# Optimization experiments

Measured on AMD Instinct MI355X. Metric: run time of the kernel, lower is better.

## Reference

```python
import jax, jax.numpy as jnp
import numpy as np

B, T, W, F, H = 4, 1024, 33, 512, 8
DK = F // H


def setup_inputs() -> dict:
    key = jax.random.key(0)
    ks = jax.random.split(key, 12)
    s = 1.0 / np.sqrt(F)
    return {
        "query": jax.random.normal(ks[0], (B, T, F), jnp.float32),
        "key": jax.random.normal(ks[1], (B, T, W, F), jnp.float32),
        "value": jax.random.normal(ks[2], (B, T, W, F), jnp.float32),
        "mask": jnp.ones((B, 1, T, W), jnp.int32),
        "Wq": jax.random.uniform(ks[3], (F, F), jnp.float32, -s, s),
        "bq": jax.random.uniform(ks[4], (F,), jnp.float32, -s, s),
        "Wk": jax.random.uniform(ks[5], (F, F), jnp.float32, -s, s),
        "bk": jax.random.uniform(ks[6], (F,), jnp.float32, -s, s),
        "Wv": jax.random.uniform(ks[7], (F, F), jnp.float32, -s, s),
        "bv": jax.random.uniform(ks[8], (F,), jnp.float32, -s, s),
        "Wo": jax.random.uniform(ks[9], (F, F), jnp.float32, -s, s),
        "bo": jax.random.uniform(ks[10], (F,), jnp.float32, -s, s),
    }


def reference(query, key, value, mask, Wq, bq, Wk, bk, Wv, bv, Wo, bo):
    b, t, w, f = key.shape
    # projections
    q = (query @ Wq + bq).reshape(b, t, H, DK)            # (B,T,H,Dk)
    k = (key @ Wk + bk).reshape(b, t, w, H, DK)           # (B,T,W,H,Dk)
    v = (value @ Wv + bv).reshape(b, t, w, H, DK)
    # windowed scores: each query attends to its own window of keys
    scores = jnp.einsum("bthd,btwhd->bhtw", q, k) / jnp.sqrt(jnp.asarray(DK, q.dtype))
    m = (mask == 0)                                       # (B,1,T,W), broadcasts over heads
    min_value = jnp.finfo(scores.dtype).min
    scores = jnp.where(m, min_value, scores)
    attn = jax.nn.softmax(scores, axis=-1)
    attn = jnp.where(m, 0.0, attn)                        # (B,H,T,W)
    x = jnp.einsum("bhtw,btwhd->bthd", attn, v).reshape(b, t, H * DK)
    return x @ Wo + bo
```

## Files before the change

kernel.cpp:

```cpp
#include <hip/hip_runtime.h>
#include <hip/hip_bf16.h>
#include <cstdint>

#define B_ 4
#define T_ 1024
#define W_ 33
#define F_ 512
#define H_ 8
#define DK_ 64

typedef __attribute__((ext_vector_type(8))) short short8;
typedef __attribute__((ext_vector_type(4))) float f32x4;

__device__ __forceinline__ float b2f(ushort u) {
  return __uint_as_float(((uint32_t)u) << 16);
}
__device__ __forceinline__ ushort f2b(float f) {
  union { __hip_bfloat16 b; ushort u; } cv;
  cv.b = __float2bfloat16(f);
  return cv.u;
}

__global__ void convert_w(const float* __restrict__ Wq, const float* __restrict__ Wk,
                          const float* __restrict__ Wv, const float* __restrict__ Wo,
                          ushort* __restrict__ out)
{
  int which = blockIdx.y;
  const float* src = (which == 0) ? Wq : (which == 1) ? Wk : (which == 2) ? Wv : Wo;
  ushort* dst = out + (size_t)which * 262144;
  int idx = blockIdx.x * 256 + threadIdx.x;
  int e = idx & 7;
  int l = (idx >> 3) & 63;
  float v;
  if (which == 1) {
    int kc  = (idx >> 9) & 1;
    int ntf = (idx >> 10) & 31;
    int h   = idx >> 15;
    v = src[(size_t)(ntf * 16 + (l & 15)) * 512 + h * 64 + kc * 32 + ((l >> 4) << 3) + e];
  } else {
    int kc = (idx >> 9) & 15;
    int nt = idx >> 13;
    int k = kc * 32 + ((l >> 4) << 3) + e;
    int n = (nt << 4) + (l & 15);
    v = src[(size_t)k * 512 + n];
  }
  dst[idx] = f2b(v);
}

template<bool A_F32, bool OUT_F32>
__global__ __launch_bounds__(256, 2)
void gemm_pipe(const void* __restrict__ Ap, const ushort* __restrict__ Bf,
               const float* __restrict__ bias, void* __restrict__ Cp, float scale)
{
  __shared__ ushort lA[3][128 * 64];

  const int tid  = threadIdx.x;
  const int lane = tid & 63;
  const int wid  = tid >> 6;
  const int wr   = wid >> 1, wc = wid & 1;
  const int lrow = lane & 15;
  const int lk8  = (lane >> 4) * 8;

  int nwg  = gridDim.x;
  int xcd  = blockIdx.x & 7;
  int slot = blockIdx.x >> 3;
  int q8   = nwg >> 3, r8 = nwg & 7;
  int base = (xcd < r8) ? xcd * (q8 + 1) : r8 * (q8 + 1) + (xcd - r8) * q8;
  int L    = base + slot;
  int bm   = L >> 2;
  int bn   = L & 3;

  int lb_[4];
  size_t asrc_[4];
#pragma unroll
  for (int p = 0; p < 4; ++p) {
    int c   = p * 256 + tid;
    int row = c >> 3;
    int kc  = (c & 7) * 8;
    lb_[p]  = (row * 128 + kc * 2) ^ ((row & 7) << 4);
    asrc_[p] = (size_t)(bm * 128 + row) * 512 + kc;
  }

  const int ntb = bn * 8 + wc * 4;

  float4 P0a0[4], P0a1[4], P1a0[4], P1a1[4];
  short8 P0r[4], P1r[4];
  short8 Q0[8], Q1[8];

  auto issueA = [&](int ks, float4 (&d0)[4], float4 (&d1)[4], short8 (&dr)[4]) {
#pragma unroll
    for (int p = 0; p < 4; ++p) {
      if (A_F32) {
        const float* src = (const float*)Ap + asrc_[p] + ks * 64;
        d0[p] = *(const float4*)src;
        d1[p] = *(const float4*)(src + 4);
      } else {
        dr[p] = *(const short8*)((const ushort*)Ap + asrc_[p] + ks * 64);
      }
    }
  };
  auto lwriteA = [&](int buf, float4 (&d0)[4], float4 (&d1)[4], short8 (&dr)[4]) {
#pragma unroll
    for (int p = 0; p < 4; ++p) {
      short8 hv;
      if (A_F32) {
        hv[0] = (short)f2b(d0[p].x); hv[1] = (short)f2b(d0[p].y);
        hv[2] = (short)f2b(d0[p].z); hv[3] = (short)f2b(d0[p].w);
        hv[4] = (short)f2b(d1[p].x); hv[5] = (short)f2b(d1[p].y);
        hv[6] = (short)f2b(d1[p].z); hv[7] = (short)f2b(d1[p].w);
      } else {
        hv = dr[p];
      }
      *(short8*)((char*)lA[buf] + lb_[p]) = hv;
    }
  };
  auto loadB = [&](int ks, short8 (&dq)[8]) {
#pragma unroll
    for (int kk = 0; kk < 2; ++kk)
#pragma unroll
      for (int nf = 0; nf < 4; ++nf)
        dq[kk * 4 + nf] = *(const short8*)(Bf +
            (((size_t)(ntb + nf) * 16 + ks * 2 + kk) * 64 + lane) * 8);
  };

  f32x4 acc[4][4];
#pragma unroll
  for (int i = 0; i < 4; ++i)
#pragma unroll
    for (int j = 0; j < 4; ++j) acc[i][j] = {0.f, 0.f, 0.f, 0.f};

  auto computeStep = [&](int buf, short8 (&dq)[8]) {
#pragma unroll
    for (int kk = 0; kk < 2; ++kk) {
      short8 af[4];
#pragma unroll
      for (int mf = 0; mf < 4; ++mf) {
        int row = wr * 64 + mf * 16 + lrow;
        int off = (row * 128 + (kk * 32 + lk8) * 2) ^ ((row & 7) << 4);
        af[mf] = *(const short8*)((const char*)lA[buf] + off);
      }
#pragma unroll
      for (int mf = 0; mf < 4; ++mf)
#pragma unroll
        for (int nf = 0; nf < 4; ++nf)
          acc[mf][nf] = __builtin_amdgcn_mfma_f32_16x16x32_bf16(af[mf], dq[kk * 4 + nf], acc[mf][nf], 0, 0, 0);
    }
  };

  issueA(0, P0a0, P0a1, P0r);
  issueA(1, P1a0, P1a1, P1r);
  loadB(0, Q0);
  lwriteA(0, P0a0, P0a1, P0r);
  __syncthreads();

#define GSTEP(T, PWa0, PWa1, PWr, PIa0, PIa1, PIr, QW, QR)                    \
  {                                                                           \
    if ((T) + 1 < 8) lwriteA(((T) + 1) % 3, PWa0, PWa1, PWr);                 \
    if ((T) + 2 < 8) issueA((T) + 2, PIa0, PIa1, PIr);                        \
    if ((T) + 1 < 8) loadB((T) + 1, QW);                                      \
    computeStep((T) % 3, QR);                                                 \
    if ((T) < 7) __syncthreads();                                             \
  }

  GSTEP(0, P1a0, P1a1, P1r, P0a0, P0a1, P0r, Q1, Q0)
  GSTEP(1, P0a0, P0a1, P0r, P1a0, P1a1, P1r, Q0, Q1)
  GSTEP(2, P1a0, P1a1, P1r, P0a0, P0a1, P0r, Q1, Q0)
  GSTEP(3, P0a0, P0a1, P0r, P1a0, P1a1, P1r, Q0, Q1)
  GSTEP(4, P1a0, P1a1, P1r, P0a0, P0a1, P0r, Q1, Q0)
  GSTEP(5, P0a0, P0a1, P0r, P1a0, P1a1, P1r, Q0, Q1)
  GSTEP(6, P1a0, P1a1, P1r, P0a0, P0a1, P0r, Q1, Q0)
  GSTEP(7, P0a0, P0a1, P0r, P1a0, P1a1, P1r, Q0, Q1)
#undef GSTEP

  float bs[4];
#pragma unroll
  for (int nf = 0; nf < 4; ++nf)
    bs[nf] = bias[bn * 128 + wc * 64 + nf * 16 + lrow];

  const int r0 = (lane >> 4) * 4;
#pragma unroll
  for (int mf = 0; mf < 4; ++mf) {
#pragma unroll
    for (int nf = 0; nf < 4; ++nf) {
      int gcol = bn * 128 + wc * 64 + nf * 16 + lrow;
#pragma unroll
      for (int r = 0; r < 4; ++r) {
        int grow = bm * 128 + wr * 64 + mf * 16 + r0 + r;
        float val = (acc[mf][nf][r] + bs[nf]) * scale;
        if (OUT_F32) ((float*)Cp)[(size_t)grow * 512 + gcol] = val;
        else         ((ushort*)Cp)[(size_t)grow * 512 + gcol] = f2b(val);
      }
    }
  }
}

__global__ __launch_bounds__(256, 4)
void r_gemm(const ushort* __restrict__ q, const ushort* __restrict__ WkR,
            ushort* __restrict__ R)
{
  const int tid  = threadIdx.x;
  const int lane = tid & 63;
  const int wid  = tid >> 6;
  const int lr   = lane & 15;
  const int l8   = (lane >> 4) * 8;
  const int mg   = blockIdx.x >> 1;
  const int nh   = blockIdx.x & 1;
  const int h    = blockIdx.y;
  const int m0   = mg * 64;
  const int ntb  = nh * 16 + wid * 4;

  short8 af[2][4], bg[2][4];
#pragma unroll
  for (int ks = 0; ks < 2; ++ks)
#pragma unroll
    for (int mf = 0; mf < 4; ++mf)
      af[ks][mf] = *(const short8*)(q + (size_t)(m0 + mf * 16 + lr) * 512 + h * 64 + ks * 32 + l8);
#pragma unroll
  for (int ks = 0; ks < 2; ++ks)
#pragma unroll
    for (int nf = 0; nf < 4; ++nf)
      bg[ks][nf] = *(const short8*)(WkR + ((size_t)((h * 32 + ntb + nf) * 2 + ks) * 64 + lane) * 8);

  f32x4 acc[4][4];
#pragma unroll
  for (int i = 0; i < 4; ++i)
#pragma unroll
    for (int j = 0; j < 4; ++j) acc[i][j] = {0.f, 0.f, 0.f, 0.f};

#pragma unroll
  for (int ks = 0; ks < 2; ++ks)
#pragma unroll
    for (int mf = 0; mf < 4; ++mf)
#pragma unroll
      for (int nf = 0; nf < 4; ++nf)
        acc[mf][nf] = __builtin_amdgcn_mfma_f32_16x16x32_bf16(af[ks][mf], bg[ks][nf], acc[mf][nf], 0, 0, 0);

  const int rr = (lane >> 4) * 4;
#pragma unroll
  for (int mf = 0; mf < 4; ++mf)
#pragma unroll
    for (int nf = 0; nf < 4; ++nf) {
      int col = nh * 256 + wid * 64 + nf * 16 + lr;
#pragma unroll
      for (int r = 0; r < 4; ++r) {
        int row = m0 + mf * 16 + rr + r;
        R[((size_t)row * 8 + h) * 512 + col] = f2b(acc[mf][nf][r]);
      }
    }
}

__global__ __launch_bounds__(256, 6)
void attn_scores(const float* __restrict__ key, const ushort* __restrict__ R,
                 const int* __restrict__ mask, float* __restrict__ probs,
                 float* __restrict__ asum)
{
  __shared__ float la[W_][8];

  const int tid  = threadIdx.x;
  const int lane = tid & 63;
  const int wv   = tid >> 6;
  const int bt   = blockIdx.x;

  int mreg = 0;
  if (lane < W_) mreg = mask[(size_t)bt * W_ + lane];
  unsigned long long mbits = __ballot(mreg != 0);

  const int h0 = wv * 2;
  float Rf[2][8];
  {
    const ushort* Rb = R + (size_t)bt * 4096 + lane * 8;
    short8 rv0 = *(const short8*)(Rb + (size_t)h0 * 512);
    short8 rv1 = *(const short8*)(Rb + (size_t)(h0 + 1) * 512);
#pragma unroll
    for (int j = 0; j < 8; ++j) {
      Rf[0][j] = b2f((ushort)rv0[j]);
      Rf[1][j] = b2f((ushort)rv1[j]);
    }
  }

  const float* kb = key + (size_t)bt * (W_ * 512) + lane * 8;
#pragma unroll 3
  for (int w = 0; w < W_; ++w) {
    float4 ka = *(const float4*)(kb + (size_t)w * 512);
    float4 kc = *(const float4*)(kb + (size_t)w * 512 + 4);
    float s0 = ka.x * Rf[0][0] + ka.y * Rf[0][1] + ka.z * Rf[0][2] + ka.w * Rf[0][3]
             + kc.x * Rf[0][4] + kc.y * Rf[0][5] + kc.z * Rf[0][6] + kc.w * Rf[0][7];
    float s1 = ka.x * Rf[1][0] + ka.y * Rf[1][1] + ka.z * Rf[1][2] + ka.w * Rf[1][3]
             + kc.x * Rf[1][4] + kc.y * Rf[1][5] + kc.z * Rf[1][6] + kc.w * Rf[1][7];
#pragma unroll
    for (int m = 1; m < 64; m <<= 1) {
      s0 += __shfl_xor(s0, m, 64);
      s1 += __shfl_xor(s1, m, 64);
    }
    float t = (lane == 0) ? s0 : s1;
    float e = ((mbits >> w) & 1ull) ? __expf(t) : 0.f;
    if (lane < 2) la[w][h0 + lane] = e;
  }
  __syncthreads();

  const int hh = tid & 7;
  float ss = 0.f;
#pragma unroll
  for (int w = 0; w < W_; ++w) ss += la[w][hh];
  float inv = (mbits != 0ull) ? 1.f / ss : 0.f;

  for (int t = tid; t < H_ * W_; t += 256) {
    int w = t >> 3;
    probs[(size_t)bt * 264 + t] = la[w][hh] * inv;
  }
  if (tid < H_)
    asum[(size_t)bt * H_ + tid] = (mbits != 0ull) ? 1.f : 0.f;
}

__global__ __launch_bounds__(256, 8)
void attn_pv(const float* __restrict__ value, const float* __restrict__ probs,
             ushort* __restrict__ g)
{
  __shared__ float lp[W_ * 8];

  const int tid = threadIdx.x;
  const int bt  = blockIdx.x;

  for (int c = tid; c < W_ * 8; c += 256)
    lp[c] = probs[(size_t)bt * 264 + c];
  __syncthreads();

  const float* vb = value + (size_t)bt * (W_ * 512) + tid * 2;
  float gg0[8], gg1[8];
#pragma unroll
  for (int h = 0; h < 8; ++h) { gg0[h] = 0.f; gg1[h] = 0.f; }

#pragma unroll
  for (int w = 0; w < W_; ++w) {
    float2 v = *(const float2*)(vb + (size_t)w * 512);
    f32x4 a0 = *(const f32x4*)&lp[w * 8];
    f32x4 a1 = *(const f32x4*)&lp[w * 8 + 4];
    gg0[0] += a0[0] * v.x; gg1[0] += a0[0] * v.y;
    gg0[1] += a0[1] * v.x; gg1[1] += a0[1] * v.y;
    gg0[2] += a0[2] * v.x; gg1[2] += a0[2] * v.y;
    gg0[3] += a0[3] * v.x; gg1[3] += a0[3] * v.y;
    gg0[4] += a1[0] * v.x; gg1[4] += a1[0] * v.y;
    gg0[5] += a1[1] * v.x; gg1[5] += a1[1] * v.y;
    gg0[6] += a1[2] * v.x; gg1[6] += a1[2] * v.y;
    gg0[7] += a1[3] * v.x; gg1[7] += a1[3] * v.y;
  }

  ushort* gb = g + (size_t)bt * 4096 + tid * 2;
#pragma unroll
  for (int h = 0; h < 8; ++h) {
    ushort2 pk;
    pk.x = f2b(gg0[h]);
    pk.y = f2b(gg1[h]);
    *(ushort2*)(gb + h * 512) = pk;
  }
}

__global__ __launch_bounds__(256, 2)
void x_proj(const ushort* __restrict__ g, const ushort* __restrict__ WtV,
            const float* __restrict__ bv, const float* __restrict__ asum,
            ushort* __restrict__ x)
{
  const int tid  = threadIdx.x;
  const int lane = tid & 63;
  const int wid  = tid >> 6;
  const int lr   = lane & 15;
  const int l8   = (lane >> 4) * 8;
  const int h    = blockIdx.y;
  const int m0   = blockIdx.x * 256 + wid * 64;
  const int ntb  = h * 4;

  f32x4 acc[4][4];
#pragma unroll
  for (int i = 0; i < 4; ++i)
#pragma unroll
    for (int j = 0; j < 4; ++j) acc[i][j] = {0.f, 0.f, 0.f, 0.f};

  short8 a0[4], a1[4], b0[4], b1[4];

  auto issue = [&](int ks, short8 (&A)[4], short8 (&Bq)[4]) {
#pragma unroll
    for (int mf = 0; mf < 4; ++mf)
      A[mf] = *(const short8*)(g + ((size_t)(m0 + mf * 16 + lr) * 8 + h) * 512 + ks * 32 + l8);
#pragma unroll
    for (int nf = 0; nf < 4; ++nf)
      Bq[nf] = *(const short8*)(WtV + ((size_t)((ntb + nf) * 16 + ks) * 64 + lane) * 8);
  };
  auto step = [&](short8 (&A)[4], short8 (&Bq)[4]) {
#pragma unroll
    for (int mf = 0; mf < 4; ++mf)
#pragma unroll
      for (int nf = 0; nf < 4; ++nf)
        acc[mf][nf] = __builtin_amdgcn_mfma_f32_16x16x32_bf16(A[mf], Bq[nf], acc[mf][nf], 0, 0, 0);
  };

  issue(0, a0, b0);
  issue(1, a1, b1);
#pragma unroll 1
  for (int ks = 0; ks < 16; ks += 2) {
    step(a0, b0);
    if (ks + 2 < 16) issue(ks + 2, a0, b0);
    step(a1, b1);
    if (ks + 3 < 16) issue(ks + 3, a1, b1);
  }

  float bvv[4];
#pragma unroll
  for (int nf = 0; nf < 4; ++nf)
    bvv[nf] = bv[h * 64 + nf * 16 + lr];

  const int rr = (lane >> 4) * 4;
#pragma unroll
  for (int mf = 0; mf < 4; ++mf)
#pragma unroll
    for (int nf = 0; nf < 4; ++nf) {
      int col = h * 64 + nf * 16 + lr;
#pragma unroll
      for (int r = 0; r < 4; ++r) {
        int row = m0 + mf * 16 + rr + r;
        float val = acc[mf][nf][r] + asum[(size_t)row * 8 + h] * bvv[nf];
        x[(size_t)row * 512 + col] = f2b(val);
      }
    }
}

extern "C" void kernel_launch(void* const* d_in, const int* in_sizes, int n_in,
                              void* d_out, int out_size, void* d_ws, size_t ws_size,
                              hipStream_t stream)
{
  const float* query = (const float*)d_in[0];
  const float* key   = (const float*)d_in[1];
  const float* value = (const float*)d_in[2];
  const int*   mask  = (const int*)d_in[3];
  const float* Wq    = (const float*)d_in[4];
  const float* bq    = (const float*)d_in[5];
  const float* Wk    = (const float*)d_in[6];
  const float* bk    = (const float*)d_in[7];
  const float* Wv    = (const float*)d_in[8];
  const float* bv    = (const float*)d_in[9];
  const float* Wo    = (const float*)d_in[10];
  const float* bo    = (const float*)d_in[11];
  (void)bk;

  char* ws = (char*)d_ws;
  ushort* Wt    = (ushort*)ws;
  ushort* WtQ   = Wt;
  ushort* WkR   = Wt + 262144;
  ushort* WtV   = Wt + 524288;
  ushort* WtO   = Wt + 786432;
  ushort* qws   = (ushort*)(ws + (size_t)2  * 1024 * 1024);
  ushort* Rws   = (ushort*)(ws + (size_t)6  * 1024 * 1024);
  ushort* gws   = (ushort*)(ws + (size_t)38 * 1024 * 1024);
  float*  asum  = (float*) (ws + (size_t)70 * 1024 * 1024);
  float*  probs = (float*) (ws + (size_t)70 * 1024 * 1024 + 256 * 1024);
  ushort* xws   = qws;

  convert_w<<<dim3(1024, 4), 256, 0, stream>>>(Wq, Wk, Wv, Wo, Wt);

  gemm_pipe<true, false><<<dim3(128, 1), 256, 0, stream>>>(query, WtQ, bq, qws, 0.125f);

  r_gemm<<<dim3(128, 8), 256, 0, stream>>>(qws, WkR, Rws);

  attn_scores<<<dim3(B_ * T_, 1), 256, 0, stream>>>(key, Rws, mask, probs, asum);

  attn_pv<<<dim3(B_ * T_, 1), 256, 0, stream>>>(value, probs, gws);

  x_proj<<<dim3(16, 8), 256, 0, stream>>>(gws, WtV, bv, asum, xws);

  gemm_pipe<false, true><<<dim3(128, 1), 256, 0, stream>>>(xws, WtO, bo, d_out, 1.0f);
}
```

Measured before the change: 211.5 us.

## Split window rows across waves in attn_scores and reduce all heads jointly

The scores kernel used to give each wave two heads and stream all 33 key rows, so every key row was loaded by all four waves. Now each wave keeps all 8 heads' query projections in registers and takes a strided subset of window rows. Each key element is therefore loaded once per block, and every load is issued up front. The cross-lane reduction uses a select-and-butterfly pattern that merges 8 head sums into one shuffle chain, cutting total shuffles. Register use rises sharply, so the launch-bounds occupancy hint drops from 6 to 3 blocks.

```diff
diff --git a/kernel.cpp b/kernel.cpp
--- a/kernel.cpp
+++ b/kernel.cpp
@@ -249,7 +249,7 @@
     }
 }
 
-__global__ __launch_bounds__(256, 6)
+__global__ __launch_bounds__(256, 3)
 void attn_scores(const float* __restrict__ key, const ushort* __restrict__ R,
                  const int* __restrict__ mask, float* __restrict__ probs,
                  float* __restrict__ asum)
@@ -265,37 +265,71 @@
   if (lane < W_) mreg = mask[(size_t)bt * W_ + lane];
   unsigned long long mbits = __ballot(mreg != 0);
 
-  const int h0 = wv * 2;
-  float Rf[2][8];
+  float Rf[8][8];
   {
     const ushort* Rb = R + (size_t)bt * 4096 + lane * 8;
-    short8 rv0 = *(const short8*)(Rb + (size_t)h0 * 512);
-    short8 rv1 = *(const short8*)(Rb + (size_t)(h0 + 1) * 512);
-#pragma unroll
-    for (int j = 0; j < 8; ++j) {
-      Rf[0][j] = b2f((ushort)rv0[j]);
-      Rf[1][j] = b2f((ushort)rv1[j]);
+#pragma unroll
+    for (int h = 0; h < 8; ++h) {
+      short8 rv = *(const short8*)(Rb + h * 512);
+#pragma unroll
+      for (int j = 0; j < 8; ++j) Rf[h][j] = b2f((ushort)rv[j]);
     }
   }
 
   const float* kb = key + (size_t)bt * (W_ * 512) + lane * 8;
-#pragma unroll 3
-  for (int w = 0; w < W_; ++w) {
-    float4 ka = *(const float4*)(kb + (size_t)w * 512);
-    float4 kc = *(const float4*)(kb + (size_t)w * 512 + 4);
-    float s0 = ka.x * Rf[0][0] + ka.y * Rf[0][1] + ka.z * Rf[0][2] + ka.w * Rf[0][3]
-             + kc.x * Rf[0][4] + kc.y * Rf[0][5] + kc.z * Rf[0][6] + kc.w * Rf[0][7];
-    float s1 = ka.x * Rf[1][0] + ka.y * Rf[1][1] + ka.z * Rf[1][2] + ka.w * Rf[1][3]
-             + kc.x * Rf[1][4] + kc.y * Rf[1][5] + kc.z * Rf[1][6] + kc.w * Rf[1][7];
-#pragma unroll
-    for (int m = 1; m < 64; m <<= 1) {
-      s0 += __shfl_xor(s0, m, 64);
-      s1 += __shfl_xor(s1, m, 64);
-    }
-    float t = (lane == 0) ? s0 : s1;
+  float kA[4][8], kB[5][8];
+#pragma unroll
+  for (int jj = 0; jj < 4; ++jj) {
+    int w = wv + jj * 4;
+    float4 a = *(const float4*)(kb + (size_t)w * 512);
+    float4 b = *(const float4*)(kb + (size_t)w * 512 + 4);
+    kA[jj][0] = a.x; kA[jj][1] = a.y; kA[jj][2] = a.z; kA[jj][3] = a.w;
+    kA[jj][4] = b.x; kA[jj][5] = b.y; kA[jj][6] = b.z; kA[jj][7] = b.w;
+  }
+#pragma unroll
+  for (int jj = 0; jj < 4; ++jj) {
+    int w = wv + 16 + jj * 4;
+    float4 a = *(const float4*)(kb + (size_t)w * 512);
+    float4 b = *(const float4*)(kb + (size_t)w * 512 + 4);
+    kB[jj][0] = a.x; kB[jj][1] = a.y; kB[jj][2] = a.z; kB[jj][3] = a.w;
+    kB[jj][4] = b.x; kB[jj][5] = b.y; kB[jj][6] = b.z; kB[jj][7] = b.w;
+  }
+  if (wv == 0) {
+    float4 a = *(const float4*)(kb + (size_t)32 * 512);
+    float4 b = *(const float4*)(kb + (size_t)32 * 512 + 4);
+    kB[4][0] = a.x; kB[4][1] = a.y; kB[4][2] = a.z; kB[4][3] = a.w;
+    kB[4][4] = b.x; kB[4][5] = b.y; kB[4][6] = b.z; kB[4][7] = b.w;
+  }
+
+  auto scoreRow = [&](const float (&kr)[8], int w) {
+    float s[8];
+#pragma unroll
+    for (int h = 0; h < 8; ++h)
+      s[h] = kr[0] * Rf[h][0] + kr[1] * Rf[h][1] + kr[2] * Rf[h][2] + kr[3] * Rf[h][3]
+           + kr[4] * Rf[h][4] + kr[5] * Rf[h][5] + kr[6] * Rf[h][6] + kr[7] * Rf[h][7];
+#pragma unroll
+    for (int m = 1; m <= 4; m <<= 1)
+#pragma unroll
+      for (int h = 0; h < 8; ++h) s[h] += __shfl_xor(s[h], m, 64);
+    float ta = (lane & 1) ? s[1] : s[0];
+    float tb = (lane & 1) ? s[3] : s[2];
+    float tc = (lane & 1) ? s[5] : s[4];
+    float td = (lane & 1) ? s[7] : s[6];
+    float ua = (lane & 2) ? tb : ta;
+    float ub = (lane & 2) ? td : tc;
+    float t  = (lane & 4) ? ub : ua;
+    t += __shfl_xor(t, 8, 64);
+    t += __shfl_xor(t, 16, 64);
+    t += __shfl_xor(t, 32, 64);
     float e = ((mbits >> w) & 1ull) ? __expf(t) : 0.f;
-    if (lane < 2) la[w][h0 + lane] = e;
-  }
+    if (lane < 8) la[w][lane] = e;
+  };
+
+#pragma unroll
+  for (int jj = 0; jj < 4; ++jj) scoreRow(kA[jj], wv + jj * 4);
+#pragma unroll
+  for (int jj = 0; jj < 4; ++jj) scoreRow(kB[jj], wv + 16 + jj * 4);
+  if (wv == 0) scoreRow(kB[4], 32);
   __syncthreads();
 
   const int hh = tid & 7;
```

Measured after the change: 180.8 us. 1.17x faster.
